# Performance work log

Measured on AMD Instinct MI355X. Metric: run time of the kernel, lower is better.

The kernel has to match this reference:

```python
import jax, jax.numpy as jnp
import numpy as np

EPS = 1e-5

def _pairwise_sqdist(A):
    # (N,P,C) -> (N,P,P) squared euclidean distances
    r = jnp.sum(A * A, axis=2, keepdims=True)          # (N,P,1)
    m = jnp.einsum('npc,nqc->npq', A, A)               # (N,P,P)
    return r - 2.0 * m + jnp.swapaxes(r, 1, 2)

def _bn(x, gamma, beta, axes):
    # training-mode batch norm (biased variance), per-channel on last axis
    mu = jnp.mean(x, axis=axes, keepdims=True)
    var = jnp.var(x, axis=axes, keepdims=True)
    return (x - mu) * jax.lax.rsqrt(var + EPS) * gamma + beta

def setup_inputs() -> dict:
    key = jax.random.key(0)
    ks = jax.random.split(key, 12)
    N, P, Ccoord, Cin = 128, 512, 2, 64
    chans = [64, 64, 64]
    inp = {
        'points': jax.random.normal(ks[0], (N, P, Ccoord), dtype=jnp.float32),
        'features': jax.random.normal(ks[1], (N, P, Cin), dtype=jnp.float32),
    }
    in_ch = 2 * Cin
    for i, out_ch in enumerate(chans):
        inp[f'W{i}'] = jax.random.normal(ks[2 + i], (out_ch, in_ch), dtype=jnp.float32) * (1.0 / np.sqrt(in_ch))
        inp[f'g{i}'] = jnp.ones((out_ch,), dtype=jnp.float32)
        inp[f'b{i}'] = jnp.zeros((out_ch,), dtype=jnp.float32)
        in_ch = out_ch
    inp['scW'] = jax.random.normal(ks[5], (chans[-1], Cin), dtype=jnp.float32) * (1.0 / np.sqrt(Cin))
    inp['scg'] = jnp.ones((chans[-1],), dtype=jnp.float32)
    inp['scb'] = jnp.zeros((chans[-1],), dtype=jnp.float32)
    return inp

K = 16

def reference(points, features, W0, g0, b0, W1, g1, b1, W2, g2, b2, scW, scg, scb):
    # --- KNN graph construction ---
    D = _pairwise_sqdist(points)                          # (N,P,P)
    _, idx = jax.lax.top_k(-D, K + 1)                     # (N,P,K+1)
    idx = idx[:, :, 1:]                                   # drop self -> (N,P,K)
    # --- gather neighbor features ---
    knn_feats = jax.vmap(lambda f, i: f[i])(features, idx)  # (N,P,K,C)
    center = features[:, :, None, :]                      # (N,P,1,C)
    x = jnp.concatenate([jnp.broadcast_to(center, knn_feats.shape),
                         knn_feats - center], axis=-1)    # (N,P,K,2C)
    # --- per-edge 1x1 conv + BN + ReLU stack ---
    for W, g, b in ((W0, g0, b0), (W1, g1, b1), (W2, g2, b2)):
        x = jnp.einsum('npkc,oc->npko', x, W)
        x = jax.nn.relu(_bn(x, g, b, axes=(0, 1, 2)))
    # --- pool over neighbors ---
    x = jnp.mean(x, axis=2)                               # (N,P,Cout)
    # --- shortcut path ---
    sc = jnp.einsum('npc,oc->npo', features, scW)         # (N,P,Cout)
    sc = jax.nn.relu(_bn(sc, scg, scb, axes=(0, 1)))
    return x + sc                                         # (N,P,Cout)
```

## Files before the change

### kernel.cpp

```cpp
#include <hip/hip_runtime.h>
#include <stdint.h>

typedef unsigned short u16;
typedef __attribute__((ext_vector_type(8))) short bf8v;
typedef __attribute__((ext_vector_type(4))) float f32x4;

#define NB   128
#define NP   512
#define KNN  16
#define CH   64
#define NPB  8
#define GPH  (NB * NP / NPB)
#define GRID_MLP 1024
#define GPB  8
#define SLOTS 512

#define OFF_IDX   0
#define OFF_PART  0x400000
#define PART_BYTES (4 * SLOTS * 2 * 64 * 4)
#define OFF_BN    0x500000
#define OFF_WN    0x500800
#define OFF_WC    0x502800
#define OFF_W1B   0x504800
#define OFF_W2B   0x506800
#define OFF_SCWB  0x508800
#define OFF_FB16  0x600000
#define OFF_Y1    0x1000000
#define Y1_BYTES  ((size_t)GPH * 256 * 32 * 2)

__device__ __forceinline__ u16 f2bf(float f) {
    union { float f; unsigned u; } v; v.f = f;
    unsigned r = v.u + 0x7fffu + ((v.u >> 16) & 1u);
    return (u16)(r >> 16);
}
__device__ __forceinline__ float bf2f(u16 b) {
    union { unsigned u; float f; } v; v.u = ((unsigned)b) << 16;
    return v.f;
}
struct alignas(16) US8 { u16 v[8]; };
__device__ __forceinline__ US8 pack8(float4 f0, float4 f1) {
    US8 u;
    u.v[0]=f2bf(f0.x); u.v[1]=f2bf(f0.y); u.v[2]=f2bf(f0.z); u.v[3]=f2bf(f0.w);
    u.v[4]=f2bf(f1.x); u.v[5]=f2bf(f1.y); u.v[6]=f2bf(f1.z); u.v[7]=f2bf(f1.w);
    return u;
}

__global__ void prep_weights(const float* __restrict__ W0, const float* __restrict__ W1,
                             const float* __restrict__ W2, const float* __restrict__ scW,
                             u16* Wn, u16* Wc, u16* W1b, u16* W2b, u16* scWb) {
    int i = blockIdx.x * 256 + threadIdx.x;
    if (i < 4096) {
        int o = i >> 6, c = i & 63;
        float a = W0[o * 128 + c], b = W0[o * 128 + 64 + c];
        Wc[i] = f2bf(a - b);
        Wn[i] = f2bf(b);
        W1b[i]  = f2bf(W1[i]);
        W2b[i]  = f2bf(W2[i]);
        scWb[i] = f2bf(scW[i]);
    }
}

__global__ void feats_to_bf16(const float* __restrict__ feats, u16* __restrict__ fb16) {
    size_t i = ((size_t)blockIdx.x * 256 + threadIdx.x) * 8;
    float4 f0 = *(const float4*)(feats + i);
    float4 f1 = *(const float4*)(feats + i + 4);
    *(US8*)(fb16 + i) = pack8(f0, f1);
}

#define INS32(ub, qq) do { if ((ub) < d16) {                                  \
    bool c00=(ub)<d00, c01=(ub)<d01, c02=(ub)<d02, c03=(ub)<d03,              \
         c04=(ub)<d04, c05=(ub)<d05, c06=(ub)<d06, c07=(ub)<d07,              \
         c08=(ub)<d08, c09=(ub)<d09, c10=(ub)<d10, c11=(ub)<d11,              \
         c12=(ub)<d12, c13=(ub)<d13, c14=(ub)<d14, c15=(ub)<d15;              \
    d16 = c15 ? d15 : (ub);                 i16 = c15 ? i15 : (qq);           \
    d15 = c14 ? d14 : (c15 ? (ub) : d15);   i15 = c14 ? i14 : (c15 ? (qq) : i15); \
    d14 = c13 ? d13 : (c14 ? (ub) : d14);   i14 = c13 ? i13 : (c14 ? (qq) : i14); \
    d13 = c12 ? d12 : (c13 ? (ub) : d13);   i13 = c12 ? i12 : (c13 ? (qq) : i13); \
    d12 = c11 ? d11 : (c12 ? (ub) : d12);   i12 = c11 ? i11 : (c12 ? (qq) : i12); \
    d11 = c10 ? d10 : (c11 ? (ub) : d11);   i11 = c10 ? i10 : (c11 ? (qq) : i11); \
    d10 = c09 ? d09 : (c10 ? (ub) : d10);   i10 = c09 ? i09 : (c10 ? (qq) : i10); \
    d09 = c08 ? d08 : (c09 ? (ub) : d09);   i09 = c08 ? i08 : (c09 ? (qq) : i09); \
    d08 = c07 ? d07 : (c08 ? (ub) : d08);   i08 = c07 ? i07 : (c08 ? (qq) : i08); \
    d07 = c06 ? d06 : (c07 ? (ub) : d07);   i07 = c06 ? i06 : (c07 ? (qq) : i07); \
    d06 = c05 ? d05 : (c06 ? (ub) : d06);   i06 = c05 ? i05 : (c06 ? (qq) : i06); \
    d05 = c04 ? d04 : (c05 ? (ub) : d05);   i05 = c04 ? i04 : (c05 ? (qq) : i05); \
    d04 = c03 ? d03 : (c04 ? (ub) : d04);   i04 = c03 ? i03 : (c04 ? (qq) : i04); \
    d03 = c02 ? d02 : (c03 ? (ub) : d03);   i03 = c02 ? i02 : (c03 ? (qq) : i03); \
    d02 = c01 ? d01 : (c02 ? (ub) : d02);   i02 = c01 ? i01 : (c02 ? (qq) : i02); \
    d01 = c00 ? d00 : (c01 ? (ub) : d01);   i01 = c00 ? i00 : (c01 ? (qq) : i01); \
    d00 = c00 ? (ub) : d00;                 i00 = c00 ? (qq) : i00;           \
} } while (0)

__global__ __launch_bounds__(256)
void knn_kernel(const float* __restrict__ pts, int* __restrict__ idx) {
#pragma clang fp contract(off)
    __shared__ __align__(16) float4 sp[NP];
    const int tid = threadIdx.x;
    const int n = blockIdx.x >> 1;
    const float* pb = pts + (size_t)n * NP * 2;
    for (int i = tid; i < NP; i += 256) {
        float x = pb[i * 2], y = pb[i * 2 + 1];
        float r = x * x + y * y;
        sp[i] = make_float4(x, y, r, 0.f);
    }
    __syncthreads();
    const int p = ((blockIdx.x & 1) << 8) + tid;
    const float xp = sp[p].x, yp = sp[p].y, rp = sp[p].z;

    unsigned d00=~0u,d01=~0u,d02=~0u,d03=~0u,d04=~0u,d05=~0u,d06=~0u,d07=~0u,
             d08=~0u,d09=~0u,d10=~0u,d11=~0u,d12=~0u,d13=~0u,d14=~0u,d15=~0u,
             d16=~0u;
    unsigned i00=0,i01=0,i02=0,i03=0,i04=0,i05=0,i06=0,i07=0,
             i08=0,i09=0,i10=0,i11=0,i12=0,i13=0,i14=0,i15=0,i16=0;

    for (int q = 0; q < NP; ++q) {
        float4 sq = sp[q];
        float m = xp * sq.x + yp * sq.y;
        float d = (rp - 2.0f * m) + sq.z;
        unsigned int ub = __float_as_uint(d);
        ub = (ub & 0x80000000u) ? ~ub : (ub | 0x80000000u);
        INS32(ub, (unsigned)q);
    }
    int* ob = idx + ((size_t)n * NP + p) * KNN;
    ob[ 0] = (int)i01;  ob[ 1] = (int)i02;  ob[ 2] = (int)i03;  ob[ 3] = (int)i04;
    ob[ 4] = (int)i05;  ob[ 5] = (int)i06;  ob[ 6] = (int)i07;  ob[ 7] = (int)i08;
    ob[ 8] = (int)i09;  ob[ 9] = (int)i10;  ob[10] = (int)i11;  ob[11] = (int)i12;
    ob[12] = (int)i13;  ob[13] = (int)i14;  ob[14] = (int)i15;  ob[15] = (int)i16;
}

__global__ void finalize_bn(const float* __restrict__ part, float* __restrict__ bn,
                            const float* g0, const float* b0, const float* g1,
                            const float* b1, const float* g2, const float* b2,
                            const float* scg, const float* scb, int mapA, int mapB) {
    int L = (blockIdx.x == 0) ? mapA : mapB;
    int o = threadIdx.x;
    const float* g = (L == 0) ? g0 : (L == 1) ? g1 : (L == 2) ? g2 : scg;
    const float* b = (L == 0) ? b0 : (L == 1) ? b1 : (L == 2) ? b2 : scb;
    float cnt = (L == 3) ? (float)(NB * NP) : (float)(NB * NP * KNN);
    float s = 0.f, ss = 0.f;
    for (int slot = 0; slot < SLOTS; ++slot) {
        s  += part[((L * SLOTS + slot) * 2 + 0) * 64 + o];
        ss += part[((L * SLOTS + slot) * 2 + 1) * 64 + o];
    }
    float mu  = s / cnt;
    float var = fmaxf(ss / cnt - mu * mu, 0.f);
    float sc  = g[o] * rsqrtf(var + 1e-5f);
    bn[L * 128 + o]      = sc;
    bn[L * 128 + 64 + o] = b[o] - mu * sc;
}

#define MFMA16(a, b, c) __builtin_amdgcn_mfma_f32_16x16x32_bf16(a, b, c, 0, 0, 0)

template <int PHASE>
__global__ __launch_bounds__(256)
void mlp_phase(const u16* __restrict__ fb16, const int* __restrict__ idx,
               const u16* __restrict__ Wn, const u16* __restrict__ Wc,
               const u16* __restrict__ W1b, const u16* __restrict__ W2b,
               const u16* __restrict__ scWb, const float* __restrict__ bn,
               float* __restrict__ part, u16* __restrict__ ybuf,
               float* __restrict__ out) {
    __shared__ char AbA[128 * 128];
    __shared__ char AbB[128 * 128];
    __shared__ char ceA[NPB * 128];
    __shared__ char ceB[NPB * 128];
    __shared__ float scsA[NPB][64];
    __shared__ float scsB[NPB][64];

    const int tid = threadIdx.x;
    const int lane = tid & 63;
    const int w = tid >> 6;
    const int l15 = lane & 15;
    const int g4 = lane >> 4;
    const int r0 = w * 32 + l15, r1 = r0 + 16;
    const int sw0 = (r0 & 7) << 4;
    const int gr_ = w * 32 + (lane >> 1);
    const int gh_ = lane & 1;
    const int gp_ = gr_ >> 4;
    const int gk_ = gr_ & 15;
    const int gsw_ = (gr_ & 7) << 4;
    const int cr_ = 2 * w + ((lane >> 4) & 1);

    for (int it = 0; it < GPB / 2; ++it) {
        const int gbA = blockIdx.x + it * (2 * GRID_MLP);
        const int gbB = gbA + GRID_MLP;
        const int nA = gbA >> 6, nB = gbB >> 6;
        const size_t rbA = (size_t)nA * NP + (gbA & 63) * NPB;
        const size_t rbB = (size_t)nB * NP + (gbB & 63) * NPB;

        f32x4 accA[2][4], accB[2][4];

        auto layer2 = [&](const u16* Wb) {
#pragma unroll
            for (int ks = 0; ks < 2; ++ks) {
                bf8v aA0 = *(const bf8v*)(AbA + r0 * 128 + ((ks * 64 + g4 * 16) ^ sw0));
                bf8v aA1 = *(const bf8v*)(AbA + r1 * 128 + ((ks * 64 + g4 * 16) ^ sw0));
                bf8v aB0 = *(const bf8v*)(AbB + r0 * 128 + ((ks * 64 + g4 * 16) ^ sw0));
                bf8v aB1 = *(const bf8v*)(AbB + r1 * 128 + ((ks * 64 + g4 * 16) ^ sw0));
#pragma unroll
                for (int ct = 0; ct < 4; ++ct) {
                    bf8v b = *(const bf8v*)((const char*)Wb + (ct * 16 + l15) * 128 + ks * 64 + g4 * 16);
                    accA[0][ct] = MFMA16(aA0, b, accA[0][ct]);
                    accA[1][ct] = MFMA16(aA1, b, accA[1][ct]);
                    accB[0][ct] = MFMA16(aB0, b, accB[0][ct]);
                    accB[1][ct] = MFMA16(aB1, b, accB[1][ct]);
                }
            }
        };
        auto layerC2 = [&](const u16* Wb) {
#pragma unroll
            for (int ks = 0; ks < 2; ++ks) {
                bf8v cA0 = *(const bf8v*)(ceA + (2 * w) * 128 + ks * 64 + g4 * 16);
                bf8v cA1 = *(const bf8v*)(ceA + (2 * w + 1) * 128 + ks * 64 + g4 * 16);
                bf8v cB0 = *(const bf8v*)(ceB + (2 * w) * 128 + ks * 64 + g4 * 16);
                bf8v cB1 = *(const bf8v*)(ceB + (2 * w + 1) * 128 + ks * 64 + g4 * 16);
#pragma unroll
                for (int ct = 0; ct < 4; ++ct) {
                    bf8v b = *(const bf8v*)((const char*)Wb + (ct * 16 + l15) * 128 + ks * 64 + g4 * 16);
                    accA[0][ct] = MFMA16(cA0, b, accA[0][ct]);
                    accA[1][ct] = MFMA16(cA1, b, accA[1][ct]);
                    accB[0][ct] = MFMA16(cB0, b, accB[0][ct]);
                    accB[1][ct] = MFMA16(cB1, b, accB[1][ct]);
                }
            }
        };
        auto store_acc = [&]() {
            u16* ya = ybuf + ((size_t)gbA * 256 + tid) * 32;
            u16* yc = ybuf + ((size_t)gbB * 256 + tid) * 32;
#pragma unroll
            for (int c4 = 0; c4 < 4; ++c4) {
                US8 ua, ub;
#pragma unroll
                for (int e = 0; e < 8; ++e) {
                    int i = c4 * 8 + e;
                    ua.v[e] = f2bf(accA[i >> 4][(i >> 2) & 3][i & 3]);
                    ub.v[e] = f2bf(accB[i >> 4][(i >> 2) & 3][i & 3]);
                }
                ((US8*)ya)[c4] = ua;
                ((US8*)yc)[c4] = ub;
            }
        };
        auto load_acc = [&]() {
            const u16* ya = ybuf + ((size_t)gbA * 256 + tid) * 32;
            const u16* yc = ybuf + ((size_t)gbB * 256 + tid) * 32;
#pragma unroll
            for (int c4 = 0; c4 < 4; ++c4) {
                US8 ua = ((const US8*)ya)[c4];
                US8 ub = ((const US8*)yc)[c4];
#pragma unroll
                for (int e = 0; e < 8; ++e) {
                    int i = c4 * 8 + e;
                    accA[i >> 4][(i >> 2) & 3][i & 3] = bf2f(ua.v[e]);
                    accB[i >> 4][(i >> 2) & 3][i & 3] = bf2f(ub.v[e]);
                }
            }
        };
        auto load_centers = [&]() {
            if (lane < 32) {
                ((uint2*)(ceA + cr_ * 128))[lane & 15] =
                    ((const uint2*)(fb16 + (rbA + cr_) * CH))[lane & 15];
                ((uint2*)(ceB + cr_ * 128))[lane & 15] =
                    ((const uint2*)(fb16 + (rbB + cr_) * CH))[lane & 15];
            }
        };
        auto stats2 = [&](int L) {
#pragma unroll
            for (int ct = 0; ct < 4; ++ct) {
                float a = 0.f, b = 0.f, c = 0.f, d = 0.f;
#pragma unroll
                for (int rt = 0; rt < 2; ++rt)
#pragma unroll
                    for (int j = 0; j < 4; ++j) {
                        float vA = accA[rt][ct][j]; a += vA; b += vA * vA;
                        float vB = accB[rt][ct][j]; c += vB; d += vB * vB;
                    }
                a += __shfl_xor(a, 16); a += __shfl_xor(a, 32);
                b += __shfl_xor(b, 16); b += __shfl_xor(b, 32);
                c += __shfl_xor(c, 16); c += __shfl_xor(c, 32);
                d += __shfl_xor(d, 16); d += __shfl_xor(d, 32);
                if (lane < 16) {
                    int sA = (gbA * 4 + w) & (SLOTS - 1);
                    int sB = (gbB * 4 + w) & (SLOTS - 1);
                    int ch = ct * 16 + lane;
                    atomicAdd(&part[((L * SLOTS + sA) * 2 + 0) * 64 + ch], a);
                    atomicAdd(&part[((L * SLOTS + sA) * 2 + 1) * 64 + ch], b);
                    atomicAdd(&part[((L * SLOTS + sB) * 2 + 0) * 64 + ch], c);
                    atomicAdd(&part[((L * SLOTS + sB) * 2 + 1) * 64 + ch], d);
                }
            }
        };
        auto bnwb2 = [&](int L) {
#pragma unroll
            for (int ct = 0; ct < 4; ++ct) {
                int ch = ct * 16 + l15;
                float sc = bn[L * 128 + ch], sh = bn[L * 128 + 64 + ch];
#pragma unroll
                for (int rt = 0; rt < 2; ++rt)
#pragma unroll
                    for (int j = 0; j < 4; ++j) {
                        int gr = w * 32 + rt * 16 + g4 * 4 + j;
                        int off = gr * 128 + ((ch * 2) ^ ((gr & 7) << 4));
                        float vA = fmaxf(fmaf(accA[rt][ct][j], sc, sh), 0.f);
                        float vB = fmaxf(fmaf(accB[rt][ct][j], sc, sh), 0.f);
                        *(u16*)(AbA + off) = f2bf(vA);
                        *(u16*)(AbB + off) = f2bf(vB);
                        accA[rt][ct][j] = 0.f;
                        accB[rt][ct][j] = 0.f;
                    }
            }
        };

        if (PHASE == 1) {
            int srcA = idx[(rbA + gp_) * KNN + gk_];
            int srcB = idx[(rbB + gp_) * KNN + gk_];
            const US8* gA = (const US8*)(fb16 + ((size_t)nA * NP + srcA) * CH + gh_ * 32);
            const US8* gB = (const US8*)(fb16 + ((size_t)nB * NP + srcB) * CH + gh_ * 32);
            US8 aq0 = gA[0], aq1 = gA[1], aq2 = gA[2], aq3 = gA[3];
            US8 bq0 = gB[0], bq1 = gB[1], bq2 = gB[2], bq3 = gB[3];
            uint2 acen = ((const uint2*)(fb16 + (rbA + cr_) * CH))[lane & 15];
            uint2 bcen = ((const uint2*)(fb16 + (rbB + cr_) * CH))[lane & 15];
            char* ra = AbA + gr_ * 128;
            *(US8*)(ra + ((gh_ * 64 +  0) ^ gsw_)) = aq0;
            *(US8*)(ra + ((gh_ * 64 + 16) ^ gsw_)) = aq1;
            *(US8*)(ra + ((gh_ * 64 + 32) ^ gsw_)) = aq2;
            *(US8*)(ra + ((gh_ * 64 + 48) ^ gsw_)) = aq3;
            char* rb = AbB + gr_ * 128;
            *(US8*)(rb + ((gh_ * 64 +  0) ^ gsw_)) = bq0;
            *(US8*)(rb + ((gh_ * 64 + 16) ^ gsw_)) = bq1;
            *(US8*)(rb + ((gh_ * 64 + 32) ^ gsw_)) = bq2;
            *(US8*)(rb + ((gh_ * 64 + 48) ^ gsw_)) = bq3;
            if (lane < 32) {
                ((uint2*)(ceA + cr_ * 128))[lane & 15] = acen;
                ((uint2*)(ceB + cr_ * 128))[lane & 15] = bcen;
            }
#pragma unroll
            for (int rt = 0; rt < 2; ++rt)
#pragma unroll
                for (int ct = 0; ct < 4; ++ct) {
                    accA[rt][ct] = (f32x4){0.f, 0.f, 0.f, 0.f};
                    accB[rt][ct] = (f32x4){0.f, 0.f, 0.f, 0.f};
                }
            layer2(Wn);
            layerC2(Wc);
            store_acc();
            stats2(0);
            f32x4 shA[4], shB[4];
#pragma unroll
            for (int ct = 0; ct < 4; ++ct) {
                shA[ct] = (f32x4){0.f, 0.f, 0.f, 0.f};
                shB[ct] = (f32x4){0.f, 0.f, 0.f, 0.f};
            }
#pragma unroll
            for (int ks = 0; ks < 2; ++ks) {
                int arow = (l15 < 2) ? (2 * w + l15) : (2 * w);
                bf8v aA = *(const bf8v*)(ceA + arow * 128 + ks * 64 + g4 * 16);
                bf8v aB = *(const bf8v*)(ceB + arow * 128 + ks * 64 + g4 * 16);
#pragma unroll
                for (int ct = 0; ct < 4; ++ct) {
                    bf8v b = *(const bf8v*)((const char*)scWb + (ct * 16 + l15) * 128 + ks * 64 + g4 * 16);
                    shA[ct] = MFMA16(aA, b, shA[ct]);
                    shB[ct] = MFMA16(aB, b, shB[ct]);
                }
            }
#pragma unroll
            for (int ct = 0; ct < 4; ++ct) {
                float uA = (g4 == 0) ? shA[ct][0] : 0.f;
                float vA = (g4 == 0) ? shA[ct][1] : 0.f;
                float uB = (g4 == 0) ? shB[ct][0] : 0.f;
                float vB = (g4 == 0) ? shB[ct][1] : 0.f;
                float a = uA + vA, b = uA * uA + vA * vA;
                float c = uB + vB, d = uB * uB + vB * vB;
                a += __shfl_xor(a, 16); a += __shfl_xor(a, 32);
                b += __shfl_xor(b, 16); b += __shfl_xor(b, 32);
                c += __shfl_xor(c, 16); c += __shfl_xor(c, 32);
                d += __shfl_xor(d, 16); d += __shfl_xor(d, 32);
                if (lane < 16) {
                    int sA = (gbA * 4 + w) & (SLOTS - 1);
                    int sB = (gbB * 4 + w) & (SLOTS - 1);
                    int ch = ct * 16 + lane;
                    atomicAdd(&part[((3 * SLOTS + sA) * 2 + 0) * 64 + ch], a);
                    atomicAdd(&part[((3 * SLOTS + sA) * 2 + 1) * 64 + ch], b);
                    atomicAdd(&part[((3 * SLOTS + sB) * 2 + 0) * 64 + ch], c);
                    atomicAdd(&part[((3 * SLOTS + sB) * 2 + 1) * 64 + ch], d);
                }
            }
            continue;
        }

        if (PHASE == 2) {
            load_acc();
            bnwb2(0);
            layer2(W1b);
            store_acc();
            stats2(1);
            continue;
        }
        if (PHASE == 3) {
            load_acc();
            bnwb2(1);
            layer2(W2b);
            store_acc();
            stats2(2);
            continue;
        }

        load_acc();
        load_centers();
        {
            float m0A[4], m1A[4], m0B[4], m1B[4];
#pragma unroll
            for (int ct = 0; ct < 4; ++ct) {
                int ch = ct * 16 + l15;
                float sc = bn[2 * 128 + ch], sh = bn[2 * 128 + 64 + ch];
                float ma = 0.f, mb = 0.f, mc = 0.f, md = 0.f;
#pragma unroll
                for (int j = 0; j < 4; ++j) {
                    ma += fmaxf(fmaf(accA[0][ct][j], sc, sh), 0.f);
                    mb += fmaxf(fmaf(accA[1][ct][j], sc, sh), 0.f);
                    mc += fmaxf(fmaf(accB[0][ct][j], sc, sh), 0.f);
                    md += fmaxf(fmaf(accB[1][ct][j], sc, sh), 0.f);
                }
                ma += __shfl_xor(ma, 16); ma += __shfl_xor(ma, 32);
                mb += __shfl_xor(mb, 16); mb += __shfl_xor(mb, 32);
                mc += __shfl_xor(mc, 16); mc += __shfl_xor(mc, 32);
                md += __shfl_xor(md, 16); md += __shfl_xor(md, 32);
                m0A[ct] = ma; m1A[ct] = mb; m0B[ct] = mc; m1B[ct] = md;
            }
            f32x4 shA[4], shB[4];
#pragma unroll
            for (int ct = 0; ct < 4; ++ct) {
                shA[ct] = (f32x4){0.f, 0.f, 0.f, 0.f};
                shB[ct] = (f32x4){0.f, 0.f, 0.f, 0.f};
            }
#pragma unroll
            for (int ks = 0; ks < 2; ++ks) {
                int arow = (l15 < 2) ? (2 * w + l15) : (2 * w);
                bf8v aA = *(const bf8v*)(ceA + arow * 128 + ks * 64 + g4 * 16);
                bf8v aB = *(const bf8v*)(ceB + arow * 128 + ks * 64 + g4 * 16);
#pragma unroll
                for (int ct = 0; ct < 4; ++ct) {
                    bf8v b = *(const bf8v*)((const char*)scWb + (ct * 16 + l15) * 128 + ks * 64 + g4 * 16);
                    shA[ct] = MFMA16(aA, b, shA[ct]);
                    shB[ct] = MFMA16(aB, b, shB[ct]);
                }
            }
            if (g4 == 0) {
#pragma unroll
                for (int ct = 0; ct < 4; ++ct) {
                    int ch = ct * 16 + l15;
                    float s3 = bn[3 * 128 + ch], h3 = bn[3 * 128 + 64 + ch];
                    scsA[2 * w + 0][ch] = fmaxf(fmaf(shA[ct][0], s3, h3), 0.f);
                    scsA[2 * w + 1][ch] = fmaxf(fmaf(shA[ct][1], s3, h3), 0.f);
                    scsB[2 * w + 0][ch] = fmaxf(fmaf(shB[ct][0], s3, h3), 0.f);
                    scsB[2 * w + 1][ch] = fmaxf(fmaf(shB[ct][1], s3, h3), 0.f);
                }
            }
            int ph = g4 >> 1;
            int p = 2 * w + ph;
            int cb2 = g4 & 1;
            int ch0 = (cb2 * 2) * 16 + l15;
            int ch1 = ch0 + 16;
            {
                float lo0 = cb2 ? m0A[2] : m0A[0], hi0 = cb2 ? m1A[2] : m1A[0];
                float lo1 = cb2 ? m0A[3] : m0A[1], hi1 = cb2 ? m1A[3] : m1A[1];
                float mva = ph ? hi0 : lo0;
                float mvb = ph ? hi1 : lo1;
                float* ob = out + (rbA + p) * CH;
                ob[ch0] = mva * 0.0625f + scsA[p][ch0];
                ob[ch1] = mvb * 0.0625f + scsA[p][ch1];
            }
            {
                float lo0 = cb2 ? m0B[2] : m0B[0], hi0 = cb2 ? m1B[2] : m1B[0];
                float lo1 = cb2 ? m0B[3] : m0B[1], hi1 = cb2 ? m1B[3] : m1B[1];
                float mva = ph ? hi0 : lo0;
                float mvb = ph ? hi1 : lo1;
                float* ob = out + (rbB + p) * CH;
                ob[ch0] = mva * 0.0625f + scsB[p][ch0];
                ob[ch1] = mvb * 0.0625f + scsB[p][ch1];
            }
        }
    }
}

extern "C" void kernel_launch(void* const* d_in, const int* in_sizes, int n_in,
                              void* d_out, int out_size, void* d_ws, size_t ws_size,
                              hipStream_t stream) {
    const float* points = (const float*)d_in[0];
    const float* feats  = (const float*)d_in[1];
    const float* W0  = (const float*)d_in[2];
    const float* g0  = (const float*)d_in[3];
    const float* b0  = (const float*)d_in[4];
    const float* W1  = (const float*)d_in[5];
    const float* g1  = (const float*)d_in[6];
    const float* b1  = (const float*)d_in[7];
    const float* W2  = (const float*)d_in[8];
    const float* g2  = (const float*)d_in[9];
    const float* b2  = (const float*)d_in[10];
    const float* scW = (const float*)d_in[11];
    const float* scg = (const float*)d_in[12];
    const float* scb = (const float*)d_in[13];
    float* out = (float*)d_out;

    char* ws = (char*)d_ws;
    int*   idx  = (int*)(ws + OFF_IDX);
    float* part = (float*)(ws + OFF_PART);
    float* bn   = (float*)(ws + OFF_BN);
    u16*   Wn   = (u16*)(ws + OFF_WN);
    u16*   Wc   = (u16*)(ws + OFF_WC);
    u16*   W1b  = (u16*)(ws + OFF_W1B);
    u16*   W2b  = (u16*)(ws + OFF_W2B);
    u16*   scWb = (u16*)(ws + OFF_SCWB);
    u16*   fb16 = (u16*)(ws + OFF_FB16);
    u16*   y1   = (u16*)(ws + OFF_Y1);

    hipMemsetAsync(part, 0, PART_BYTES, stream);
    prep_weights<<<16, 256, 0, stream>>>(W0, W1, W2, scW, Wn, Wc, W1b, W2b, scWb);
    feats_to_bf16<<<2048, 256, 0, stream>>>(feats, fb16);
    knn_kernel<<<NB * 2, 256, 0, stream>>>(points, idx);

    mlp_phase<1><<<GRID_MLP, 256, 0, stream>>>(fb16, idx, Wn, Wc, W1b, W2b, scWb, bn, part, y1, out);
    finalize_bn<<<2, 64, 0, stream>>>(part, bn, g0, b0, g1, b1, g2, b2, scg, scb, 0, 3);
    mlp_phase<2><<<GRID_MLP, 256, 0, stream>>>(fb16, idx, Wn, Wc, W1b, W2b, scWb, bn, part, y1, out);
    finalize_bn<<<1, 64, 0, stream>>>(part, bn, g0, b0, g1, b1, g2, b2, scg, scb, 1, 1);
    mlp_phase<3><<<GRID_MLP, 256, 0, stream>>>(fb16, idx, Wn, Wc, W1b, W2b, scWb, bn, part, y1, out);
    finalize_bn<<<1, 64, 0, stream>>>(part, bn, g0, b0, g1, b1, g2, b2, scg, scb, 2, 2);
    mlp_phase<4><<<GRID_MLP, 256, 0, stream>>>(fb16, idx, Wn, Wc, W1b, W2b, scWb, bn, part, y1, out);
}
```

Before: 453.3 us.

## Split KNN scan across query halves with merge kernel, fuse bf16 feature conversion

The KNN top-k scan is split so each block handles half the candidate points. This doubles the grid to 512 blocks for better GPU occupancy, and each thread's partial top-17 list is written to workspace. A new merge kernel combines the two partial lists per point into the final indices. The features-to-bf16 conversion is folded into the scan kernel as a grid-stride loop, which removes a separate launch. This adds an extra kernel plus global traffic for the partial lists, which reuse the y1 region before it is written.

```diff
diff --git a/kernel.cpp b/kernel.cpp
--- a/kernel.cpp
+++ b/kernel.cpp
@@ -27,6 +27,7 @@
 #define OFF_FB16  0x600000
 #define OFF_Y1    0x1000000
 #define Y1_BYTES  ((size_t)GPH * 256 * 32 * 2)
+#define OFF_KPART OFF_Y1
 
 __device__ __forceinline__ u16 f2bf(float f) {
     union { float f; unsigned u; } v; v.f = f;
@@ -58,13 +59,6 @@
         W2b[i]  = f2bf(W2[i]);
         scWb[i] = f2bf(scW[i]);
     }
-}
-
-__global__ void feats_to_bf16(const float* __restrict__ feats, u16* __restrict__ fb16) {
-    size_t i = ((size_t)blockIdx.x * 256 + threadIdx.x) * 8;
-    float4 f0 = *(const float4*)(feats + i);
-    float4 f1 = *(const float4*)(feats + i + 4);
-    *(US8*)(fb16 + i) = pack8(f0, f1);
 }
 
 #define INS32(ub, qq) do { if ((ub) < d16) {                                  \
@@ -91,37 +85,80 @@
     d00 = c00 ? (ub) : d00;                 i00 = c00 ? (qq) : i00;           \
 } } while (0)
 
+#define KDECL unsigned d00=~0u,d01=~0u,d02=~0u,d03=~0u,d04=~0u,d05=~0u,       \
+    d06=~0u,d07=~0u,d08=~0u,d09=~0u,d10=~0u,d11=~0u,d12=~0u,d13=~0u,          \
+    d14=~0u,d15=~0u,d16=~0u;                                                  \
+    unsigned i00=0,i01=0,i02=0,i03=0,i04=0,i05=0,i06=0,i07=0,                 \
+    i08=0,i09=0,i10=0,i11=0,i12=0,i13=0,i14=0,i15=0,i16=0
+
 __global__ __launch_bounds__(256)
-void knn_kernel(const float* __restrict__ pts, int* __restrict__ idx) {
+void knn_scan(const float* __restrict__ pts, const float* __restrict__ feats,
+              u16* __restrict__ fb16, unsigned* __restrict__ kpart) {
 #pragma clang fp contract(off)
-    __shared__ __align__(16) float4 sp[NP];
+    __shared__ __align__(16) float4 sp[256];
     const int tid = threadIdx.x;
-    const int n = blockIdx.x >> 1;
+    {
+        const size_t nv = (size_t)NB * NP * CH / 8;
+        for (size_t i = (size_t)blockIdx.x * 256 + tid; i < nv; i += (size_t)gridDim.x * 256) {
+            float4 f0 = ((const float4*)feats)[i * 2];
+            float4 f1 = ((const float4*)feats)[i * 2 + 1];
+            ((US8*)fb16)[i] = pack8(f0, f1);
+        }
+    }
+    const int b = blockIdx.x;
+    const int n = b >> 2;
+    const int ph = (b >> 1) & 1;
+    const int qh = b & 1;
     const float* pb = pts + (size_t)n * NP * 2;
-    for (int i = tid; i < NP; i += 256) {
+    {
+        int i = qh * 256 + tid;
         float x = pb[i * 2], y = pb[i * 2 + 1];
         float r = x * x + y * y;
-        sp[i] = make_float4(x, y, r, 0.f);
+        sp[tid] = make_float4(x, y, r, 0.f);
     }
     __syncthreads();
-    const int p = ((blockIdx.x & 1) << 8) + tid;
-    const float xp = sp[p].x, yp = sp[p].y, rp = sp[p].z;
-
-    unsigned d00=~0u,d01=~0u,d02=~0u,d03=~0u,d04=~0u,d05=~0u,d06=~0u,d07=~0u,
-             d08=~0u,d09=~0u,d10=~0u,d11=~0u,d12=~0u,d13=~0u,d14=~0u,d15=~0u,
-             d16=~0u;
-    unsigned i00=0,i01=0,i02=0,i03=0,i04=0,i05=0,i06=0,i07=0,
-             i08=0,i09=0,i10=0,i11=0,i12=0,i13=0,i14=0,i15=0,i16=0;
-
-    for (int q = 0; q < NP; ++q) {
-        float4 sq = sp[q];
+    const int p = ph * 256 + tid;
+    float xp = pb[p * 2], yp = pb[p * 2 + 1];
+    float rp = xp * xp + yp * yp;
+
+    KDECL;
+    const int q0 = qh << 8;
+    for (int t = 0; t < 256; ++t) {
+        float4 sq = sp[t];
         float m = xp * sq.x + yp * sq.y;
         float d = (rp - 2.0f * m) + sq.z;
         unsigned int ub = __float_as_uint(d);
         ub = (ub & 0x80000000u) ? ~ub : (ub | 0x80000000u);
-        INS32(ub, (unsigned)q);
-    }
-    int* ob = idx + ((size_t)n * NP + p) * KNN;
+        INS32(ub, (unsigned)(q0 + t));
+    }
+    unsigned* pp = kpart + (((size_t)(n * NP + p)) * 2 + qh) * 34;
+    pp[ 0]=d00; pp[ 1]=d01; pp[ 2]=d02; pp[ 3]=d03; pp[ 4]=d04; pp[ 5]=d05;
+    pp[ 6]=d06; pp[ 7]=d07; pp[ 8]=d08; pp[ 9]=d09; pp[10]=d10; pp[11]=d11;
+    pp[12]=d12; pp[13]=d13; pp[14]=d14; pp[15]=d15; pp[16]=d16;
+    pp[17]=i00; pp[18]=i01; pp[19]=i02; pp[20]=i03; pp[21]=i04; pp[22]=i05;
+    pp[23]=i06; pp[24]=i07; pp[25]=i08; pp[26]=i09; pp[27]=i10; pp[28]=i11;
+    pp[29]=i12; pp[30]=i13; pp[31]=i14; pp[32]=i15; pp[33]=i16;
+}
+
+__global__ __launch_bounds__(256)
+void knn_merge(const unsigned* __restrict__ kpart, int* __restrict__ idx) {
+    const size_t pt = (size_t)blockIdx.x * 256 + threadIdx.x;
+    const unsigned* p0 = kpart + (pt * 2 + 0) * 34;
+    const unsigned* p1 = kpart + (pt * 2 + 1) * 34;
+    unsigned d00=p0[0], d01=p0[1], d02=p0[2], d03=p0[3], d04=p0[4],
+             d05=p0[5], d06=p0[6], d07=p0[7], d08=p0[8], d09=p0[9],
+             d10=p0[10],d11=p0[11],d12=p0[12],d13=p0[13],d14=p0[14],
+             d15=p0[15],d16=p0[16];
+    unsigned i00=p0[17],i01=p0[18],i02=p0[19],i03=p0[20],i04=p0[21],
+             i05=p0[22],i06=p0[23],i07=p0[24],i08=p0[25],i09=p0[26],
+             i10=p0[27],i11=p0[28],i12=p0[29],i13=p0[30],i14=p0[31],
+             i15=p0[32],i16=p0[33];
+#pragma unroll
+    for (int j = 0; j < 17; ++j) {
+        unsigned ub = p1[j], qq = p1[17 + j];
+        INS32(ub, qq);
+    }
+    int* ob = idx + pt * KNN;
     ob[ 0] = (int)i01;  ob[ 1] = (int)i02;  ob[ 2] = (int)i03;  ob[ 3] = (int)i04;
     ob[ 4] = (int)i05;  ob[ 5] = (int)i06;  ob[ 6] = (int)i07;  ob[ 7] = (int)i08;
     ob[ 8] = (int)i09;  ob[ 9] = (int)i10;  ob[10] = (int)i11;  ob[11] = (int)i12;
@@ -511,11 +548,12 @@
     u16*   scWb = (u16*)(ws + OFF_SCWB);
     u16*   fb16 = (u16*)(ws + OFF_FB16);
     u16*   y1   = (u16*)(ws + OFF_Y1);
+    unsigned* kp = (unsigned*)(ws + OFF_KPART);
 
     hipMemsetAsync(part, 0, PART_BYTES, stream);
     prep_weights<<<16, 256, 0, stream>>>(W0, W1, W2, scW, Wn, Wc, W1b, W2b, scWb);
-    feats_to_bf16<<<2048, 256, 0, stream>>>(feats, fb16);
-    knn_kernel<<<NB * 2, 256, 0, stream>>>(points, idx);
+    knn_scan<<<NB * 4, 256, 0, stream>>>(points, feats, fb16, kp);
+    knn_merge<<<NB * 2, 256, 0, stream>>>(kp, idx);
 
     mlp_phase<1><<<GRID_MLP, 256, 0, stream>>>(fb16, idx, Wn, Wc, W1b, W2b, scWb, bn, part, y1, out);
     finalize_bn<<<2, 64, 0, stream>>>(part, bn, g0, b0, g1, b1, g2, b2, scg, scb, 0, 3);
```

After: 433.3 us. -4.4%, faster.
